# Performance work log

Hardware: AMD Instinct MI355X
Metric: run time of the kernel (lower is better)

## Reference

```python
import jax, jax.numpy as jnp
import numpy as np

EPS = 1e-6


def _mp_match(reps, att, kernel):
    """BiMPM multi-perspective match.
    reps: (B,L,D); att: (B,L,D) or (B,1,D); kernel: (M,D).
    Returns (B,L,1+M): [tanh(sum(reps*att)), tanh(sum_d reps*kernel_m*att)].
    """
    prod = reps * att                                   # (B,L,D)
    cos = jnp.tanh(jnp.sum(prod, axis=-1, keepdims=True))   # (B,L,1)
    mp = jnp.tanh(jnp.einsum('bld,md->blm', prod, kernel))  # (B,L,M)
    return jnp.concatenate([cos, mp], axis=-1)


def setup_inputs() -> dict:
    key = jax.random.key(0)
    ks = jax.random.split(key, 12)
    B, Llt, Lrt, D, M, A = 32, 128, 128, 512, 64, 128
    H = D // 2
    u = lambda k, shape: jax.random.uniform(k, shape, jnp.float32, -0.05, 0.05)  # keras 'uniform' init
    return {
        'reps_lt': jax.random.normal(ks[0], (B, Llt, D), jnp.float32),
        'h_lt_fw': jax.random.normal(ks[1], (B, H), jnp.float32),
        'h_lt_bw': jax.random.normal(ks[2], (B, H), jnp.float32),
        'reps_rt': jax.random.normal(ks[3], (B, Lrt, D), jnp.float32),
        'h_rt_fw': jax.random.normal(ks[4], (B, H), jnp.float32),
        'h_rt_bw': jax.random.normal(ks[5], (B, H), jnp.float32),
        'kernel_full': u(ks[6], (M, D)),
        'kernel_mpool': u(ks[7], (M, D)),
        'attn_w1': u(ks[8], (D, A)),
        'diag_w': u(ks[9], (A,)),
        'kernel_att': u(ks[10], (M, D)),
        'kernel_maxatt': u(ks[11], (M, D)),
    }


def reference(reps_lt, h_lt_fw, h_lt_bw, reps_rt, h_rt_fw, h_rt_bw,
              kernel_full, kernel_mpool, attn_w1, diag_w,
              kernel_att, kernel_maxatt):
    # ---- full match: each left timestep vs last BiLSTM state of right ----
    h_rt = jnp.concatenate([h_rt_fw, h_rt_bw], axis=-1)[:, None, :]  # (B,1,D)
    full = _mp_match(reps_lt, h_rt, kernel_full)                     # (B,Ll,1+M)

    # ---- max-pooling match ----
    # t[b,r,l,m] = tanh(sum_d R[b,r,d]*K[m,d]*L[b,l,d]); max over right positions r
    r_scaled = jnp.einsum('brd,md->brmd', reps_rt, kernel_mpool)     # (B,Lr,M,D)
    t = jnp.tanh(jnp.einsum('brmd,bld->brlm', r_scaled, reps_lt))    # (B,Lr,Ll,M)
    mpool = jnp.max(t, axis=1)                                       # (B,Ll,M)

    # ---- attentive match ----
    a_lt = jnp.tanh(reps_lt @ attn_w1) * diag_w                      # (B,Ll,A)
    a_rt = jnp.tanh(reps_rt @ attn_w1)                               # (B,Lr,A)
    scores = jnp.einsum('bla,bra->blr', a_lt, a_rt)                  # (B,Ll,Lr)
    probs = jax.nn.softmax(scores, axis=-1)
    att = jnp.einsum('blr,brd->bld', probs, reps_rt)                 # (B,Ll,D)
    attentive = _mp_match(reps_lt, att, kernel_att)                  # (B,Ll,1+M)

    # ---- max-attentive match ----
    num = jnp.einsum('bld,brd->blr', reps_lt, reps_rt)
    n_lt = jnp.sqrt(jnp.maximum(jnp.sum(reps_lt * reps_lt, -1), EPS))[:, :, None]
    n_rt = jnp.sqrt(jnp.maximum(jnp.sum(reps_rt * reps_rt, -1), EPS))[:, None, :]
    rel = num / n_rt / n_lt                                          # (B,Ll,Lr)
    idx = jnp.argmax(rel, axis=2)                                    # (B,Ll) int
    max_att = jnp.take_along_axis(reps_rt, idx[:, :, None], axis=1)  # (B,Ll,D)
    maxatt = _mp_match(reps_lt, max_att, kernel_maxatt)              # (B,Ll,1+M)

    return jnp.concatenate([full, mpool, attentive, maxatt], axis=-1)  # (B,Ll,3+4M)
```

## Files before the change

### kernel.cpp

```cpp
#include <hip/hip_runtime.h>
#include <hip/hip_bf16.h>
#include <math.h>
#include <stdint.h>

typedef __attribute__((ext_vector_type(8))) short short8;
typedef __attribute__((ext_vector_type(4))) float float4v;

#define DEV static __device__ __forceinline__

DEV float bflo(unsigned int u) { union { unsigned int i; float f; } v; v.i = u << 16; return v.f; }
DEV float bfhi(unsigned int u) { union { unsigned int i; float f; } v; v.i = u & 0xffff0000u; return v.f; }
DEV unsigned short f2bf(float f) {
    union { float f; unsigned int i; } v; v.f = f;
    unsigned int x = v.i;
    return (unsigned short)((x + 0x7fffu + ((x >> 16) & 1u)) >> 16);
}
DEV unsigned int pack2(float a, float b) { return (unsigned int)f2bf(a) | ((unsigned int)f2bf(b) << 16); }
#if __has_builtin(__builtin_amdgcn_cvt_pk_bf16_f32)
DEV unsigned int pack2_fast(float a, float b) {
    typedef __attribute__((ext_vector_type(2))) short short2v;
    short2v r = __builtin_amdgcn_cvt_pk_bf16_f32(a, b);
    union { short2v s; unsigned int u; } v; v.s = r; return v.u;
}
#else
DEV unsigned int pack2_fast(float a, float b) { return pack2(a, b); }
#endif
DEV void unpack8(uint4 u, float* f) {
    f[0]=bflo(u.x); f[1]=bfhi(u.x); f[2]=bflo(u.y); f[3]=bfhi(u.y);
    f[4]=bflo(u.z); f[5]=bfhi(u.z); f[6]=bflo(u.w); f[7]=bfhi(u.w);
}

DEV void async16(const unsigned short* g, unsigned short* l) {
    __builtin_amdgcn_global_load_lds(
        (const __attribute__((address_space(1))) unsigned int*)g,
        (__attribute__((address_space(3))) unsigned int*)l, 16, 0, 0);
}

__global__ __launch_bounds__(256) void prep_kernel(const float* __restrict__ lt,
                                                   const float* __restrict__ rt,
                                                   const float* __restrict__ kf,
                                                   const float* __restrict__ kmp,
                                                   const float* __restrict__ ka,
                                                   const float* __restrict__ km,
                                                   const float* __restrict__ w1,
                                                   unsigned short* __restrict__ ltb,
                                                   unsigned short* __restrict__ rtb,
                                                   unsigned short* __restrict__ kb,
                                                   unsigned short* __restrict__ w1t,
                                                   double* __restrict__ rsq) {
    __shared__ double ws2[2][2];
    __shared__ float tile[32][33];
    int bid = blockIdx.x, t = threadIdx.x;
    if (bid < 1024) {
        bool isRt = bid >= 512;
        int base = (isRt ? (bid - 512) : bid) * 8;
        int rl = t >> 7;
        int c  = t & 127;
        const float* srcb = isRt ? rt : lt;
        unsigned short* dstb = isRt ? rtb : ltb;
        #pragma unroll
        for (int p = 0; p < 4; ++p) {
            int row = base + p * 2 + rl;
            const float* src = srcb + (size_t)row * 512;
            float4 v = *(const float4*)(src + c * 4);
            ushort4 o;
            o.x = f2bf(v.x); o.y = f2bf(v.y); o.z = f2bf(v.z); o.w = f2bf(v.w);
            *(ushort4*)(dstb + (size_t)row * 512 + c * 4) = o;
            if (isRt) {
                double s = (double)v.x * v.x + (double)v.y * v.y
                         + (double)v.z * v.z + (double)v.w * v.w;
                #pragma unroll
                for (int off = 1; off < 64; off <<= 1) s += __shfl_xor(s, off, 64);
                if ((c & 63) == 0) ws2[rl][c >> 6] = s;
                __syncthreads();
                if (c == 0) rsq[row] = 1.0 / sqrt(ws2[rl][0] + ws2[rl][1]);
                __syncthreads();
            }
        }
    } else if (bid < 1152) {
        int kbk = bid - 1024;
        int ksel = kbk >> 5;
        const float* src = (ksel == 0) ? kf : (ksel == 1) ? kmp : (ksel == 2) ? ka : km;
        int off = (kbk & 31) * 1024 + t * 4;
        float4 v = *(const float4*)(src + off);
        ushort4 o;
        o.x = f2bf(v.x); o.y = f2bf(v.y); o.z = f2bf(v.z); o.w = f2bf(v.w);
        *(ushort4*)(kb + ksel * 32768 + off) = o;
    } else {
        int b2 = bid - 1152;
        int d0 = (b2 & 15) * 32, a0 = (b2 >> 4) * 32;
        int r = t >> 5, c = t & 31;
        #pragma unroll
        for (int i = 0; i < 32; i += 8)
            tile[r + i][c] = w1[(size_t)(d0 + r + i) * 128 + a0 + c];
        __syncthreads();
        #pragma unroll
        for (int i = 0; i < 32; i += 8)
            w1t[(size_t)(a0 + r + i) * 512 + d0 + c] = f2bf(tile[c][r + i]);
    }
}

__global__ __launch_bounds__(256, 3) void uber_kernel(
        const unsigned short* __restrict__ ltb,
        const unsigned short* __restrict__ rtb,
        const unsigned short* __restrict__ kmb,
        const unsigned short* __restrict__ w1t,
        const float* __restrict__ diag,
        unsigned short* __restrict__ a_all,
        const float* __restrict__ ltf,
        const float* __restrict__ rtf,
        const double* __restrict__ rsq,
        int* __restrict__ idxout,
        float* __restrict__ out) {
    __shared__ __align__(16) unsigned char smem[52224];
    int bx = blockIdx.x;
    int t = threadIdx.x;
    int wave = t >> 6, lane = t & 63;
    int q = lane >> 4, col = lane & 15, kq = q * 8;

    if (bx < 2048) {
        int xcd = bx & 7, jj = bx >> 3;
        int b = xcd * 4 + (jj >> 6);
        int m = jj & 63;
        unsigned short (*ltS)[72] = (unsigned short(*)[72])smem;
        unsigned short* rtL = (unsigned short*)(smem + 18432);
        float (*mx)[2] = (float(*)[2])(smem + 18432 + 32768);
        int wl = wave & 1, wr = wave >> 1;
        const unsigned short* ltp = ltb + (size_t)b * 65536;
        const unsigned short* rtp = rtb + (size_t)b * 65536;
        const unsigned short* kr = kmb + (size_t)m * 512;
        int srow = t >> 3, cg8 = t & 7, cg = cg8 * 8;
        int gsw = (cg8 ^ (srow & 7)) * 8;
        int wbase = (t & ~63) * 8;

        #pragma unroll
        for (int it = 0; it < 4; ++it)
            async16(rtp + (size_t)(it * 32 + srow) * 512 + gsw,
                    rtL + it * 2048 + wbase);
        uint4 pk = *(const uint4*)(kr + cg);
        uint4 plt[4];
        #pragma unroll
        for (int it = 0; it < 4; ++it)
            plt[it] = *(const uint4*)(ltp + (size_t)(it * 32 + srow) * 512 + cg);

        float4v acc[4][4] = {};
        for (int k0i = 0; k0i < 8; ++k0i) {
            float kf8[8]; unpack8(pk, kf8);
            #pragma unroll
            for (int it = 0; it < 4; ++it) {
                int row = it * 32 + srow;
                float lf[8]; unpack8(plt[it], lf);
                uint4 s;
                s.x = pack2_fast(lf[0] * kf8[0], lf[1] * kf8[1]);
                s.y = pack2_fast(lf[2] * kf8[2], lf[3] * kf8[3]);
                s.z = pack2_fast(lf[4] * kf8[4], lf[5] * kf8[5]);
                s.w = pack2_fast(lf[6] * kf8[6], lf[7] * kf8[7]);
                *(uint4*)&ltS[row][cg] = s;
            }
            __syncthreads();
            if (k0i < 7) {
                int k0n = (k0i + 1) * 64;
                int bofs = ((k0i + 1) & 1) * 8192;
                #pragma unroll
                for (int it = 0; it < 4; ++it)
                    async16(rtp + (size_t)(it * 32 + srow) * 512 + k0n + gsw,
                            rtL + bofs + it * 2048 + wbase);
                pk = *(const uint4*)(kr + k0n + cg);
                #pragma unroll
                for (int it = 0; it < 4; ++it)
                    plt[it] = *(const uint4*)(ltp + (size_t)(it * 32 + srow) * 512 + k0n + cg);
            }
            const unsigned short* rb = rtL + (k0i & 1) * 8192;
            #pragma unroll
            for (int kk = 0; kk < 64; kk += 32) {
                short8 af[4], bfr[4];
                #pragma unroll
                for (int i = 0; i < 4; ++i)
                    af[i] = *(const short8*)&ltS[wl * 64 + i * 16 + col][kk + kq];
                #pragma unroll
                for (int j = 0; j < 4; ++j) {
                    int row = wr * 64 + j * 16 + col;
                    int slot = ((kk >> 3) + q) ^ (row & 7);
                    bfr[j] = *(const short8*)&rb[row * 64 + slot * 8];
                }
                #pragma unroll
                for (int i = 0; i < 4; ++i)
                    #pragma unroll
                    for (int j = 0; j < 4; ++j)
                        acc[i][j] = __builtin_amdgcn_mfma_f32_16x16x32_bf16(af[i], bfr[j], acc[i][j], 0, 0, 0);
            }
            __syncthreads();
        }
        #pragma unroll
        for (int i = 0; i < 4; ++i)
            #pragma unroll
            for (int ii = 0; ii < 4; ++ii) {
                float v = fmaxf(fmaxf(acc[i][0][ii], acc[i][1][ii]), fmaxf(acc[i][2][ii], acc[i][3][ii]));
                #pragma unroll
                for (int off = 1; off < 16; off <<= 1) v = fmaxf(v, __shfl_xor(v, off, 64));
                if (col == 0) mx[wl * 64 + i * 16 + q * 4 + ii][wr] = v;
            }
        __syncthreads();
        if (t < 128)
            out[((size_t)(b * 128 + t)) * 259 + 65 + m] = tanhf(fmaxf(mx[t][0], mx[t][1]));

    } else if (bx < 2560) {
        int idA = bx - 2048;
        int xcd = idA & 7, jj = idA >> 3;
        int b = xcd * 4 + (jj >> 4);
        int L0 = (jj & 15) * 8;
        float* ltS = (float*)smem;
        float* buf = (float*)(smem + 16384);
        double* dvs = (double*)(smem + 49152);
        float* wv1 = (float*)(smem + 49152 + 128);
        float* wv2 = wv1 + 16;
        int* wi1 = (int*)(wv2 + 16);
        int* wi2 = wi1 + 16;
        int* candi = wi2 + 16;
        {
            int row = t >> 5, c0 = (t & 31) * 16;
            const float* src = ltf + ((size_t)(b * 128 + L0 + row)) * 512 + c0;
            #pragma unroll
            for (int i = 0; i < 4; ++i)
                *(float4*)&ltS[row * 512 + c0 + i * 4] = *(const float4*)(src + i * 4);
        }
        int lg = t >> 7;
        int rg = (t >> 2) & 31;
        int ds = t & 3;
        float acc[4][4] = {{0.f}};
        for (int p = 0; p < 8; ++p) {
            __syncthreads();
            {
                int row = t >> 1, c0 = (t & 1) * 32;
                const float* src = rtf + ((size_t)(b * 128 + row)) * 512 + p * 64 + c0;
                float f[32];
                #pragma unroll
                for (int i = 0; i < 8; ++i)
                    *(float4*)&f[i * 4] = *(const float4*)(src + i * 4);
                int base = row * 64;
                #pragma unroll
                for (int gg = 0; gg < 4; ++gg) {
                    int g = (t & 1) * 4 + gg;
                    int o = ((g ^ (row & 7)) * 8);
                    #pragma unroll
                    for (int k = 0; k < 8; ++k) buf[base + o + k] = f[gg * 8 + k];
                }
            }
            __syncthreads();
            #pragma unroll
            for (int sub = 0; sub < 2; ++sub) {
                int dloc = ds * 16 + sub * 8;
                int dglob = p * 64 + dloc;
                float a[4][8];
                #pragma unroll
                for (int i = 0; i < 4; ++i)
                    #pragma unroll
                    for (int k = 0; k < 8; ++k) a[i][k] = ltS[(lg * 4 + i) * 512 + dglob + k];
                int g = dloc >> 3;
                #pragma unroll
                for (int j = 0; j < 4; ++j) {
                    int r = rg + j * 32;
                    const float* rp = &buf[r * 64 + ((g ^ (r & 7)) * 8)];
                    float rv[8];
                    #pragma unroll
                    for (int k = 0; k < 8; ++k) rv[k] = rp[k];
                    #pragma unroll
                    for (int i = 0; i < 4; ++i)
                        #pragma unroll
                        for (int k = 0; k < 8; ++k)
                            acc[i][j] = fmaf(a[i][k], rv[k], acc[i][j]);
                }
            }
        }
        #pragma unroll
        for (int i = 0; i < 4; ++i)
            #pragma unroll
            for (int j = 0; j < 4; ++j) {
                acc[i][j] += __shfl_xor(acc[i][j], 1, 64);
                acc[i][j] += __shfl_xor(acc[i][j], 2, 64);
            }
        float v1[4], v2[4]; int i1[4], i2[4];
        #pragma unroll
        for (int i = 0; i < 4; ++i) {
            v1[i] = -3.0e38f; v2[i] = -3.0e38f; i1[i] = 0; i2[i] = 1;
            #pragma unroll
            for (int j = 0; j < 4; ++j) {
                int r = rg + j * 32;
                float s = acc[i][j] * (float)rsq[b * 128 + r];
                if (s > v1[i]) { v2[i] = v1[i]; i2[i] = i1[i]; v1[i] = s; i1[i] = r; }
                else if (s > v2[i]) { v2[i] = s; i2[i] = r; }
            }
        }
        #pragma unroll
        for (int off = 4; off < 64; off <<= 1) {
            #pragma unroll
            for (int i = 0; i < 4; ++i) {
                float u1 = __shfl_xor(v1[i], off, 64); int j1 = __shfl_xor(i1[i], off, 64);
                float u2 = __shfl_xor(v2[i], off, 64); int j2 = __shfl_xor(i2[i], off, 64);
                if (u1 > v1[i]) {
                    float ov = v1[i]; int oi = i1[i];
                    v1[i] = u1; i1[i] = j1;
                    if (u2 > ov) { v2[i] = u2; i2[i] = j2; } else { v2[i] = ov; i2[i] = oi; }
                } else if (u1 > v2[i]) { v2[i] = u1; i2[i] = j1; }
            }
        }
        if (lane == 0) {
            #pragma unroll
            for (int i = 0; i < 4; ++i) {
                int l = lg * 4 + i, h = wave & 1;
                wv1[l * 2 + h] = v1[i]; wi1[l * 2 + h] = i1[i];
                wv2[l * 2 + h] = v2[i]; wi2[l * 2 + h] = i2[i];
            }
        }
        __syncthreads();
        if (t < 8) {
            float a1 = wv1[t * 2], a2 = wv2[t * 2]; int ai1 = wi1[t * 2], ai2 = wi2[t * 2];
            float b1 = wv1[t * 2 + 1], b2 = wv2[t * 2 + 1]; int bi1 = wi1[t * 2 + 1], bi2 = wi2[t * 2 + 1];
            int ri1, ri2;
            if (b1 > a1) {
                ri1 = bi1;
                if (b2 > a1) { ri2 = bi2; } else { ri2 = ai1; }
            } else {
                ri1 = ai1;
                if (b1 > a2) { ri2 = bi1; } else { ri2 = ai2; }
            }
            candi[t * 2] = ri1; candi[t * 2 + 1] = ri2;
            (void)a2; (void)b2; (void)ai2; (void)bi2;
        }
        __syncthreads();
        {
            int dotid = t >> 4;
            int sub = t & 15;
            int l = dotid >> 1, c = dotid & 1;
            int r = candi[l * 2 + c];
            const float* lrow = ltf + ((size_t)(b * 128 + L0 + l)) * 512;
            const float* rrow = rtf + ((size_t)(b * 128 + r)) * 512;
            double s = 0.0;
            #pragma unroll 8
            for (int k = 0; k < 32; ++k) {
                int d = sub * 32 + k;
                s = fma((double)lrow[d], (double)rrow[d], s);
            }
            #pragma unroll
            for (int off = 1; off < 16; off <<= 1) s += __shfl_xor(s, off, 64);
            if (sub == 0) dvs[l * 2 + c] = s * rsq[b * 128 + r];
        }
        __syncthreads();
        if (t < 8) {
            int ia = candi[t * 2], ib = candi[t * 2 + 1];
            double va = dvs[t * 2], vb = dvs[t * 2 + 1];
            int res = (vb > va || (vb == va && ib < ia)) ? ib : ia;
            idxout[b * 128 + L0 + t] = res;
        }

    } else {
        int R0 = (bx - 2560) * 32;
        unsigned short (*aS)[72] = (unsigned short(*)[72])smem;
        unsigned short (*bS)[72] = (unsigned short(*)[72])(smem + 4608);
        float* diagS = (float*)(smem + 4608 + 18432);
        int wl = wave & 1, wr = wave >> 1;
        if (t < 128) diagS[t] = diag[t];
        const unsigned short* src = (R0 < 4096) ? (ltb + (size_t)R0 * 512) : (rtb + (size_t)(R0 - 4096) * 512);
        float4v acc[4] = {};
        for (int k0 = 0; k0 < 512; k0 += 64) {
            {
                int row = t >> 3, cg = (t & 7) * 8;
                *(uint4*)&aS[row][cg] = *(const uint4*)(src + (size_t)row * 512 + k0 + cg);
            }
            #pragma unroll
            for (int it = 0; it < 4; ++it) {
                int id = it * 256 + t;
                int row = id >> 3, cg = (id & 7) * 8;
                *(uint4*)&bS[row][cg] = *(const uint4*)(w1t + (size_t)row * 512 + k0 + cg);
            }
            __syncthreads();
            #pragma unroll
            for (int kk = 0; kk < 64; kk += 32) {
                short8 af = *(const short8*)&aS[wl * 16 + col][kk + kq];
                #pragma unroll
                for (int j = 0; j < 4; ++j) {
                    short8 bf = *(const short8*)&bS[wr * 64 + j * 16 + col][kk + kq];
                    acc[j] = __builtin_amdgcn_mfma_f32_16x16x32_bf16(af, bf, acc[j], 0, 0, 0);
                }
            }
            __syncthreads();
        }
        bool isLt = (R0 < 4096);
        #pragma unroll
        for (int j = 0; j < 4; ++j)
            #pragma unroll
            for (int ii = 0; ii < 4; ++ii) {
                int rowl = wl * 16 + q * 4 + ii;
                int n = wr * 64 + j * 16 + col;
                float v = tanhf(acc[j][ii]);
                if (isLt) v *= diagS[n];
                a_all[((size_t)(R0 + rowl)) * 128 + n] = f2bf(v);
            }
    }
}

__global__ __launch_bounds__(512, 1) void attn_kernel(const unsigned short* __restrict__ a_all,
                                                      const unsigned short* __restrict__ rtb,
                                                      const float* __restrict__ ltf,
                                                      const unsigned short* __restrict__ kb_att,
                                                      float* __restrict__ out) {
    int b = blockIdx.x, lg = blockIdx.y;
    int L0 = lg * 16;
    __shared__ __align__(16) unsigned short altS[16][136];
    __shared__ __align__(16) unsigned short artS[128][136];
    __shared__ __align__(16) unsigned short rtS[16][512];
    __shared__ __align__(16) unsigned short prodsF[16][520];
    __shared__ float P[16][132];
    __shared__ float pmax[16][8];
    __shared__ float psum[16][8];
    int t = threadIdx.x;
    int wave = t >> 6, lane = t & 63;
    int q = lane >> 4, col = lane & 15, kq = q * 8;

    if (t < 256) {
        int row = t >> 4, c0 = (t & 15) * 8;
        *(uint4*)&altS[row][c0] = *(const uint4*)(a_all + ((size_t)(b * 128 + L0 + row)) * 128 + c0);
    }
    {
        int row = t >> 2, c0 = (t & 3) * 32;
        const unsigned short* src = a_all + ((size_t)(4096 + b * 128 + row)) * 128 + c0;
        #pragma unroll
        for (int i = 0; i < 4; ++i)
            *(uint4*)&artS[row][c0 + i * 8] = *(const uint4*)(src + i * 8);
    }
    __syncthreads();

    float4v acc = {};
    #pragma unroll
    for (int kk = 0; kk < 128; kk += 32) {
        short8 af = *(const short8*)&altS[col][kk + kq];
        short8 bf = *(const short8*)&artS[wave * 16 + col][kk + kq];
        acc = __builtin_amdgcn_mfma_f32_16x16x32_bf16(af, bf, acc, 0, 0, 0);
    }
    float m4[4], p4[4];
    #pragma unroll
    for (int ii = 0; ii < 4; ++ii) {
        float v = acc[ii];
        #pragma unroll
        for (int off = 1; off < 16; off <<= 1) v = fmaxf(v, __shfl_xor(v, off, 64));
        m4[ii] = v;
    }
    if (col == 0) {
        #pragma unroll
        for (int ii = 0; ii < 4; ++ii) pmax[q * 4 + ii][wave] = m4[ii];
    }
    __syncthreads();
    #pragma unroll
    for (int ii = 0; ii < 4; ++ii) {
        float M = pmax[q * 4 + ii][0];
        #pragma unroll
        for (int w = 1; w < 8; ++w) M = fmaxf(M, pmax[q * 4 + ii][w]);
        p4[ii] = expf(acc[ii] - M);
        float s = p4[ii];
        #pragma unroll
        for (int off = 1; off < 16; off <<= 1) s += __shfl_xor(s, off, 64);
        m4[ii] = s;
    }
    if (col == 0) {
        #pragma unroll
        for (int ii = 0; ii < 4; ++ii) psum[q * 4 + ii][wave] = m4[ii];
    }
    __syncthreads();
    #pragma unroll
    for (int ii = 0; ii < 4; ++ii) {
        float S = psum[q * 4 + ii][0] + psum[q * 4 + ii][1] + psum[q * 4 + ii][2] + psum[q * 4 + ii][3]
                + psum[q * 4 + ii][4] + psum[q * 4 + ii][5] + psum[q * 4 + ii][6] + psum[q * 4 + ii][7];
        P[q * 4 + ii][wave * 16 + col] = p4[ii] / S;
    }

    int l = t >> 5, cd = t & 31;
    float a8[2][8] = {{0.f}};
    for (int rcb = 0; rcb < 128; rcb += 16) {
        __syncthreads();
        {
            int row = t >> 5, c0 = (t & 31) * 16;
            const unsigned short* src = rtb + ((size_t)(b * 128 + rcb + row)) * 512 + c0;
            *(uint4*)&rtS[row][c0] = *(const uint4*)src;
            *(uint4*)&rtS[row][c0 + 8] = *(const uint4*)(src + 8);
        }
        __syncthreads();
        for (int rr = 0; rr < 16; ++rr) {
            float pr = P[l][rcb + rr];
            #pragma unroll
            for (int pass = 0; pass < 2; ++pass) {
                uint4 u = *(const uint4*)&rtS[rr][pass * 256 + cd * 8];
                float f[8]; unpack8(u, f);
                #pragma unroll
                for (int k = 0; k < 8; ++k) a8[pass][k] += pr * f[k];
            }
        }
    }

    int grow = b * 128 + L0 + l;
    const float* ltrow = ltf + (size_t)grow * 512;
    float csum = 0.f;
    #pragma unroll
    for (int pass = 0; pass < 2; ++pass) {
        int d0 = pass * 256 + cd * 8;
        float lf[8];
        *(float4*)&lf[0] = *(const float4*)(ltrow + d0);
        *(float4*)&lf[4] = *(const float4*)(ltrow + d0 + 4);
        float pf[8];
        #pragma unroll
        for (int k = 0; k < 8; ++k) { pf[k] = lf[k] * a8[pass][k]; csum += pf[k]; }
        uint4 o;
        o.x = pack2(pf[0], pf[1]); o.y = pack2(pf[2], pf[3]);
        o.z = pack2(pf[4], pf[5]); o.w = pack2(pf[6], pf[7]);
        *(uint4*)&prodsF[l][d0] = o;
    }
    #pragma unroll
    for (int off = 1; off < 32; off <<= 1) csum += __shfl_xor(csum, off, 64);
    if (cd == 0) out[(size_t)grow * 259 + 129] = tanhf(csum);

    unsigned short* Ks = &artS[0][0];
    float* red = (float*)&rtS[0][0];
    for (int half = 0; half < 2; ++half) {
        __syncthreads();
        {
            int row = t >> 4, c0 = (t & 15) * 32;
            const unsigned short* src = kb_att + ((size_t)(half * 32 + row)) * 512 + c0;
            #pragma unroll
            for (int i = 0; i < 4; ++i)
                *(uint4*)&Ks[row * 520 + c0 + i * 8] = *(const uint4*)(src + i * 8);
        }
        __syncthreads();
        float4v pacc[2] = {};
        #pragma unroll
        for (int kk = 0; kk < 64; kk += 32) {
            short8 af = *(const short8*)&prodsF[col][wave * 64 + kk + kq];
            #pragma unroll
            for (int j = 0; j < 2; ++j) {
                short8 bf = *(const short8*)&Ks[(j * 16 + col) * 520 + wave * 64 + kk + kq];
                pacc[j] = __builtin_amdgcn_mfma_f32_16x16x32_bf16(af, bf, pacc[j], 0, 0, 0);
            }
        }
        #pragma unroll
        for (int j = 0; j < 2; ++j)
            #pragma unroll
            for (int ii = 0; ii < 4; ++ii)
                red[((wave * 2 + j) * 16 + q * 4 + ii) * 16 + col] = pacc[j][ii];
        __syncthreads();
        {
            int ll = t >> 5, jm = t & 31;
            int j = jm >> 4, mc = jm & 15;
            float s = 0.f;
            #pragma unroll
            for (int w = 0; w < 8; ++w) s += red[((w * 2 + j) * 16 + ll) * 16 + mc];
            out[((size_t)(b * 128 + L0 + ll)) * 259 + 130 + half * 32 + jm] = tanhf(s);
        }
    }
}

__global__ __launch_bounds__(256, 2) void mpmatch_kernel(const float* __restrict__ lt,
                                                         const unsigned short* __restrict__ rtb,
                                                         const float* __restrict__ hfw,
                                                         const float* __restrict__ hbw,
                                                         const unsigned short* __restrict__ kb,
                                                         const int* __restrict__ idxp,
                                                         float* __restrict__ out) {
    int lg = blockIdx.x, b = blockIdx.y, mode = blockIdx.z ? 2 : 0;
    int L0 = lg * 16;
    __shared__ __align__(16) unsigned short prods[16][520];
    __shared__ __align__(16) unsigned short Ks[32][520];
    __shared__ float red[4][2][16][17];
    int t = threadIdx.x;
    int wave = t >> 6, lane = t & 63;
    int q = lane >> 4, col = lane & 15, kq = q * 8;

    const unsigned short* Kp = kb + (size_t)((mode == 0) ? 0 : 3 * 32768);
    int obase = (mode == 0) ? 0 : 194;

    int l = t >> 4, c = t & 15;
    int grow = b * 128 + L0 + l;
    const float* ltrow = lt + (size_t)grow * 512;
    const unsigned short* avrow = 0;
    if (mode == 2) avrow = rtb + ((size_t)(b * 128 + idxp[grow])) * 512;

    float csum = 0.f;
    #pragma unroll
    for (int pass = 0; pass < 4; ++pass) {
        int d0 = pass * 128 + c * 8;
        float lf[8], af[8], pf[8];
        *(float4*)&lf[0] = *(const float4*)(ltrow + d0);
        *(float4*)&lf[4] = *(const float4*)(ltrow + d0 + 4);
        if (mode == 0) {
            const float* h = (d0 < 256) ? (hfw + b * 256 + d0) : (hbw + b * 256 + d0 - 256);
            *(float4*)&af[0] = *(const float4*)h;
            *(float4*)&af[4] = *(const float4*)(h + 4);
        } else {
            uint4 av = *(const uint4*)(avrow + d0);
            unpack8(av, af);
        }
        #pragma unroll
        for (int k = 0; k < 8; ++k) { pf[k] = lf[k] * af[k]; csum += pf[k]; }
        uint4 o;
        o.x = pack2(pf[0], pf[1]); o.y = pack2(pf[2], pf[3]);
        o.z = pack2(pf[4], pf[5]); o.w = pack2(pf[6], pf[7]);
        *(uint4*)&prods[l][d0] = o;
    }
    #pragma unroll
    for (int off = 1; off < 16; off <<= 1) csum += __shfl_xor(csum, off, 64);
    if (c == 0) out[(size_t)grow * 259 + obase] = tanhf(csum);

    for (int half = 0; half < 2; ++half) {
        {
            int row = t >> 3, c0 = (t & 7) * 64;
            const unsigned short* src = Kp + ((size_t)(half * 32 + row)) * 512 + c0;
            #pragma unroll
            for (int i = 0; i < 8; ++i)
                *(uint4*)&Ks[row][c0 + i * 8] = *(const uint4*)(src + i * 8);
        }
        __syncthreads();
        float4v acc[2] = {};
        #pragma unroll
        for (int kk = 0; kk < 128; kk += 32) {
            short8 af = *(const short8*)&prods[col][wave * 128 + kk + kq];
            #pragma unroll
            for (int j = 0; j < 2; ++j) {
                short8 bf = *(const short8*)&Ks[j * 16 + col][wave * 128 + kk + kq];
                acc[j] = __builtin_amdgcn_mfma_f32_16x16x32_bf16(af, bf, acc[j], 0, 0, 0);
            }
        }
        #pragma unroll
        for (int j = 0; j < 2; ++j)
            #pragma unroll
            for (int ii = 0; ii < 4; ++ii)
                red[wave][j][q * 4 + ii][col] = acc[j][ii];
        __syncthreads();
        for (int o = t; o < 512; o += 256) {
            int ll = o >> 5, jm = o & 31;
            int j = jm >> 4, mc = jm & 15;
            float s = red[0][j][ll][mc] + red[1][j][ll][mc] + red[2][j][ll][mc] + red[3][j][ll][mc];
            out[((size_t)(b * 128 + L0 + ll)) * 259 + obase + 1 + half * 32 + jm] = tanhf(s);
        }
        __syncthreads();
    }
}

extern "C" void kernel_launch(void* const* d_in, const int* in_sizes, int n_in,
                              void* d_out, int out_size, void* d_ws, size_t ws_size,
                              hipStream_t stream) {
    const float* lt  = (const float*)d_in[0];
    const float* rt  = (const float*)d_in[3];
    const float* hfw = (const float*)d_in[4];
    const float* hbw = (const float*)d_in[5];
    const float* kf  = (const float*)d_in[6];
    const float* kmp = (const float*)d_in[7];
    const float* w1  = (const float*)d_in[8];
    const float* dia = (const float*)d_in[9];
    const float* ka  = (const float*)d_in[10];
    const float* km  = (const float*)d_in[11];
    float* out = (float*)d_out;

    char* wsb = (char*)d_ws;
    unsigned short* ltb16 = (unsigned short*)(wsb);
    unsigned short* rtb16 = (unsigned short*)(wsb + 4194304);
    unsigned short* kb16  = (unsigned short*)(wsb + 8388608);
    unsigned short* w1t   = (unsigned short*)(wsb + 8650752);
    unsigned short* a_all = (unsigned short*)(wsb + 8781824);
    double*         rsq   = (double*)(wsb + 15073280);
    int*            idx   = (int*)(wsb + 15106048);

    prep_kernel<<<1216, 256, 0, stream>>>(lt, rt, kf, kmp, ka, km, w1, ltb16, rtb16, kb16, w1t, rsq);
    uber_kernel<<<2816, 256, 0, stream>>>(ltb16, rtb16, kb16 + 32768, w1t, dia, a_all,
                                          lt, rt, rsq, idx, out);
    attn_kernel<<<dim3(32, 8), 512, 0, stream>>>(a_all, rtb16, lt, kb16 + 2 * 32768, out);
    mpmatch_kernel<<<dim3(8, 32, 2), 256, 0, stream>>>(lt, rtb16, hfw, hbw, kb16, idx, out);
}
```

Before: 196.8 us.

## Merge attention and mp-match kernels into one tail launch; compute rt norms locally

Folds attn_kernel and mpmatch_kernel into a single tail_kernel that dispatches on block index, so one launch replaces two. The mp-match half now uses 512 threads and computes both 32-wide M halves in one pass. Each max-attentive block now recomputes the right-row inverse norms in shared memory, which removes the double-precision reduction and its syncs from prep_kernel. The cost is redundant norm work, a serial per-thread double loop of 256 elements, and a larger shared-memory footprint for the merged kernel.

```diff
diff --git a/kernel.cpp b/kernel.cpp
--- a/kernel.cpp
+++ b/kernel.cpp
@@ -46,9 +46,7 @@
                                                    unsigned short* __restrict__ ltb,
                                                    unsigned short* __restrict__ rtb,
                                                    unsigned short* __restrict__ kb,
-                                                   unsigned short* __restrict__ w1t,
-                                                   double* __restrict__ rsq) {
-    __shared__ double ws2[2][2];
+                                                   unsigned short* __restrict__ w1t) {
     __shared__ float tile[32][33];
     int bid = blockIdx.x, t = threadIdx.x;
     if (bid < 1024) {
@@ -66,16 +64,6 @@
             ushort4 o;
             o.x = f2bf(v.x); o.y = f2bf(v.y); o.z = f2bf(v.z); o.w = f2bf(v.w);
             *(ushort4*)(dstb + (size_t)row * 512 + c * 4) = o;
-            if (isRt) {
-                double s = (double)v.x * v.x + (double)v.y * v.y
-                         + (double)v.z * v.z + (double)v.w * v.w;
-                #pragma unroll
-                for (int off = 1; off < 64; off <<= 1) s += __shfl_xor(s, off, 64);
-                if ((c & 63) == 0) ws2[rl][c >> 6] = s;
-                __syncthreads();
-                if (c == 0) rsq[row] = 1.0 / sqrt(ws2[rl][0] + ws2[rl][1]);
-                __syncthreads();
-            }
         }
     } else if (bid < 1152) {
         int kbk = bid - 1024;
@@ -109,7 +97,6 @@
         unsigned short* __restrict__ a_all,
         const float* __restrict__ ltf,
         const float* __restrict__ rtf,
-        const double* __restrict__ rsq,
         int* __restrict__ idxout,
         float* __restrict__ out) {
     __shared__ __align__(16) unsigned char smem[52224];
@@ -217,12 +204,22 @@
         int* wi1 = (int*)(wv2 + 16);
         int* wi2 = wi1 + 16;
         int* candi = wi2 + 16;
+        double* rsqS = (double*)(smem + 50176);
         {
             int row = t >> 5, c0 = (t & 31) * 16;
             const float* src = ltf + ((size_t)(b * 128 + L0 + row)) * 512 + c0;
             #pragma unroll
             for (int i = 0; i < 4; ++i)
                 *(float4*)&ltS[row * 512 + c0 + i * 4] = *(const float4*)(src + i * 4);
+        }
+        {
+            int r = t >> 1, half = t & 1;
+            const float* rrow = rtf + ((size_t)(b * 128 + r)) * 512 + half * 256;
+            double s = 0.0;
+            #pragma unroll 4
+            for (int k = 0; k < 256; ++k) s = fma((double)rrow[k], (double)rrow[k], s);
+            s += __shfl_xor(s, 1, 64);
+            if (half == 0) rsqS[r] = 1.0 / sqrt(s);
         }
         int lg = t >> 7;
         int rg = (t >> 2) & 31;
@@ -286,7 +283,7 @@
             #pragma unroll
             for (int j = 0; j < 4; ++j) {
                 int r = rg + j * 32;
-                float s = acc[i][j] * (float)rsq[b * 128 + r];
+                float s = acc[i][j] * (float)rsqS[r];
                 if (s > v1[i]) { v2[i] = v1[i]; i2[i] = i1[i]; v1[i] = s; i1[i] = r; }
                 else if (s > v2[i]) { v2[i] = s; i2[i] = r; }
             }
@@ -343,7 +340,7 @@
             }
             #pragma unroll
             for (int off = 1; off < 16; off <<= 1) s += __shfl_xor(s, off, 64);
-            if (sub == 0) dvs[l * 2 + c] = s * rsq[b * 128 + r];
+            if (sub == 0) dvs[l * 2 + c] = s * rsqS[r];
         }
         __syncthreads();
         if (t < 8) {
@@ -399,246 +396,251 @@
     }
 }
 
-__global__ __launch_bounds__(512, 1) void attn_kernel(const unsigned short* __restrict__ a_all,
-                                                      const unsigned short* __restrict__ rtb,
-                                                      const float* __restrict__ ltf,
-                                                      const unsigned short* __restrict__ kb_att,
-                                                      float* __restrict__ out) {
-    int b = blockIdx.x, lg = blockIdx.y;
-    int L0 = lg * 16;
-    __shared__ __align__(16) unsigned short altS[16][136];
-    __shared__ __align__(16) unsigned short artS[128][136];
-    __shared__ __align__(16) unsigned short rtS[16][512];
-    __shared__ __align__(16) unsigned short prodsF[16][520];
-    __shared__ float P[16][132];
-    __shared__ float pmax[16][8];
-    __shared__ float psum[16][8];
+__global__ __launch_bounds__(512, 1) void tail_kernel(
+        const unsigned short* __restrict__ a_all,
+        const unsigned short* __restrict__ rtb,
+        const float* __restrict__ ltf,
+        const unsigned short* __restrict__ kb,
+        const float* __restrict__ hfw,
+        const float* __restrict__ hbw,
+        const int* __restrict__ idxp,
+        float* __restrict__ out) {
+    __shared__ __align__(16) unsigned char smem[99584];
+    int bx = blockIdx.x;
     int t = threadIdx.x;
     int wave = t >> 6, lane = t & 63;
     int q = lane >> 4, col = lane & 15, kq = q * 8;
 
-    if (t < 256) {
-        int row = t >> 4, c0 = (t & 15) * 8;
-        *(uint4*)&altS[row][c0] = *(const uint4*)(a_all + ((size_t)(b * 128 + L0 + row)) * 128 + c0);
-    }
-    {
-        int row = t >> 2, c0 = (t & 3) * 32;
-        const unsigned short* src = a_all + ((size_t)(4096 + b * 128 + row)) * 128 + c0;
-        #pragma unroll
-        for (int i = 0; i < 4; ++i)
-            *(uint4*)&artS[row][c0 + i * 8] = *(const uint4*)(src + i * 8);
-    }
-    __syncthreads();
-
-    float4v acc = {};
-    #pragma unroll
-    for (int kk = 0; kk < 128; kk += 32) {
-        short8 af = *(const short8*)&altS[col][kk + kq];
-        short8 bf = *(const short8*)&artS[wave * 16 + col][kk + kq];
-        acc = __builtin_amdgcn_mfma_f32_16x16x32_bf16(af, bf, acc, 0, 0, 0);
-    }
-    float m4[4], p4[4];
-    #pragma unroll
-    for (int ii = 0; ii < 4; ++ii) {
-        float v = acc[ii];
-        #pragma unroll
-        for (int off = 1; off < 16; off <<= 1) v = fmaxf(v, __shfl_xor(v, off, 64));
-        m4[ii] = v;
-    }
-    if (col == 0) {
-        #pragma unroll
-        for (int ii = 0; ii < 4; ++ii) pmax[q * 4 + ii][wave] = m4[ii];
-    }
-    __syncthreads();
-    #pragma unroll
-    for (int ii = 0; ii < 4; ++ii) {
-        float M = pmax[q * 4 + ii][0];
-        #pragma unroll
-        for (int w = 1; w < 8; ++w) M = fmaxf(M, pmax[q * 4 + ii][w]);
-        p4[ii] = expf(acc[ii] - M);
-        float s = p4[ii];
-        #pragma unroll
-        for (int off = 1; off < 16; off <<= 1) s += __shfl_xor(s, off, 64);
-        m4[ii] = s;
-    }
-    if (col == 0) {
-        #pragma unroll
-        for (int ii = 0; ii < 4; ++ii) psum[q * 4 + ii][wave] = m4[ii];
-    }
-    __syncthreads();
-    #pragma unroll
-    for (int ii = 0; ii < 4; ++ii) {
-        float S = psum[q * 4 + ii][0] + psum[q * 4 + ii][1] + psum[q * 4 + ii][2] + psum[q * 4 + ii][3]
-                + psum[q * 4 + ii][4] + psum[q * 4 + ii][5] + psum[q * 4 + ii][6] + psum[q * 4 + ii][7];
-        P[q * 4 + ii][wave * 16 + col] = p4[ii] / S;
-    }
-
-    int l = t >> 5, cd = t & 31;
-    float a8[2][8] = {{0.f}};
-    for (int rcb = 0; rcb < 128; rcb += 16) {
-        __syncthreads();
+    if (bx < 256) {
+        int b = bx & 31, lg = bx >> 5;
+        int L0 = lg * 16;
+        unsigned short (*altS)[136]  = (unsigned short(*)[136])(smem);
+        unsigned short (*artS)[136]  = (unsigned short(*)[136])(smem + 4352);
+        unsigned short (*rtS)[512]   = (unsigned short(*)[512])(smem + 39168);
+        unsigned short (*prodsF)[520]= (unsigned short(*)[520])(smem + 55552);
+        float (*P)[132]  = (float(*)[132])(smem + 72192);
+        float (*pmax)[8] = (float(*)[8])(smem + 80640);
+        float (*psum)[8] = (float(*)[8])(smem + 81152);
+        const unsigned short* kb_att = kb + 2 * 32768;
+
+        if (t < 256) {
+            int row = t >> 4, c0 = (t & 15) * 8;
+            *(uint4*)&altS[row][c0] = *(const uint4*)(a_all + ((size_t)(b * 128 + L0 + row)) * 128 + c0);
+        }
         {
-            int row = t >> 5, c0 = (t & 31) * 16;
-            const unsigned short* src = rtb + ((size_t)(b * 128 + rcb + row)) * 512 + c0;
-            *(uint4*)&rtS[row][c0] = *(const uint4*)src;
-            *(uint4*)&rtS[row][c0 + 8] = *(const uint4*)(src + 8);
-        }
-        __syncthreads();
-        for (int rr = 0; rr < 16; ++rr) {
-            float pr = P[l][rcb + rr];
-            #pragma unroll
-            for (int pass = 0; pass < 2; ++pass) {
-                uint4 u = *(const uint4*)&rtS[rr][pass * 256 + cd * 8];
-                float f[8]; unpack8(u, f);
-                #pragma unroll
-                for (int k = 0; k < 8; ++k) a8[pass][k] += pr * f[k];
-            }
-        }
-    }
-
-    int grow = b * 128 + L0 + l;
-    const float* ltrow = ltf + (size_t)grow * 512;
-    float csum = 0.f;
-    #pragma unroll
-    for (int pass = 0; pass < 2; ++pass) {
-        int d0 = pass * 256 + cd * 8;
-        float lf[8];
-        *(float4*)&lf[0] = *(const float4*)(ltrow + d0);
-        *(float4*)&lf[4] = *(const float4*)(ltrow + d0 + 4);
-        float pf[8];
-        #pragma unroll
-        for (int k = 0; k < 8; ++k) { pf[k] = lf[k] * a8[pass][k]; csum += pf[k]; }
-        uint4 o;
-        o.x = pack2(pf[0], pf[1]); o.y = pack2(pf[2], pf[3]);
-        o.z = pack2(pf[4], pf[5]); o.w = pack2(pf[6], pf[7]);
-        *(uint4*)&prodsF[l][d0] = o;
-    }
-    #pragma unroll
-    for (int off = 1; off < 32; off <<= 1) csum += __shfl_xor(csum, off, 64);
-    if (cd == 0) out[(size_t)grow * 259 + 129] = tanhf(csum);
-
-    unsigned short* Ks = &artS[0][0];
-    float* red = (float*)&rtS[0][0];
-    for (int half = 0; half < 2; ++half) {
-        __syncthreads();
+            int row = t >> 2, c0 = (t & 3) * 32;
+            const unsigned short* src = a_all + ((size_t)(4096 + b * 128 + row)) * 128 + c0;
+            #pragma unroll
+            for (int i = 0; i < 4; ++i)
+                *(uint4*)&artS[row][c0 + i * 8] = *(const uint4*)(src + i * 8);
+        }
+        __syncthreads();
+
+        float4v acc = {};
+        #pragma unroll
+        for (int kk = 0; kk < 128; kk += 32) {
+            short8 af = *(const short8*)&altS[col][kk + kq];
+            short8 bf = *(const short8*)&artS[wave * 16 + col][kk + kq];
+            acc = __builtin_amdgcn_mfma_f32_16x16x32_bf16(af, bf, acc, 0, 0, 0);
+        }
+        float m4[4], p4[4];
+        #pragma unroll
+        for (int ii = 0; ii < 4; ++ii) {
+            float v = acc[ii];
+            #pragma unroll
+            for (int off = 1; off < 16; off <<= 1) v = fmaxf(v, __shfl_xor(v, off, 64));
+            m4[ii] = v;
+        }
+        if (col == 0) {
+            #pragma unroll
+            for (int ii = 0; ii < 4; ++ii) pmax[q * 4 + ii][wave] = m4[ii];
+        }
+        __syncthreads();
+        #pragma unroll
+        for (int ii = 0; ii < 4; ++ii) {
+            float M = pmax[q * 4 + ii][0];
+            #pragma unroll
+            for (int w = 1; w < 8; ++w) M = fmaxf(M, pmax[q * 4 + ii][w]);
+            p4[ii] = expf(acc[ii] - M);
+            float s = p4[ii];
+            #pragma unroll
+            for (int off = 1; off < 16; off <<= 1) s += __shfl_xor(s, off, 64);
+            m4[ii] = s;
+        }
+        if (col == 0) {
+            #pragma unroll
+            for (int ii = 0; ii < 4; ++ii) psum[q * 4 + ii][wave] = m4[ii];
+        }
+        __syncthreads();
+        #pragma unroll
+        for (int ii = 0; ii < 4; ++ii) {
+            float S = psum[q * 4 + ii][0] + psum[q * 4 + ii][1] + psum[q * 4 + ii][2] + psum[q * 4 + ii][3]
+                    + psum[q * 4 + ii][4] + psum[q * 4 + ii][5] + psum[q * 4 + ii][6] + psum[q * 4 + ii][7];
+            P[q * 4 + ii][wave * 16 + col] = p4[ii] / S;
+        }
+
+        int l = t >> 5, cd = t & 31;
+        float a8[2][8] = {{0.f}};
+        for (int rcb = 0; rcb < 128; rcb += 16) {
+            __syncthreads();
+            {
+                int row = t >> 5, c0 = (t & 31) * 16;
+                const unsigned short* src = rtb + ((size_t)(b * 128 + rcb + row)) * 512 + c0;
+                *(uint4*)&rtS[row][c0] = *(const uint4*)src;
+                *(uint4*)&rtS[row][c0 + 8] = *(const uint4*)(src + 8);
+            }
+            __syncthreads();
+            for (int rr = 0; rr < 16; ++rr) {
+                float pr = P[l][rcb + rr];
+                #pragma unroll
+                for (int pass = 0; pass < 2; ++pass) {
+                    uint4 u = *(const uint4*)&rtS[rr][pass * 256 + cd * 8];
+                    float f[8]; unpack8(u, f);
+                    #pragma unroll
+                    for (int k = 0; k < 8; ++k) a8[pass][k] += pr * f[k];
+                }
+            }
+        }
+
+        int grow = b * 128 + L0 + l;
+        const float* ltrow = ltf + (size_t)grow * 512;
+        float csum = 0.f;
+        #pragma unroll
+        for (int pass = 0; pass < 2; ++pass) {
+            int d0 = pass * 256 + cd * 8;
+            float lf[8];
+            *(float4*)&lf[0] = *(const float4*)(ltrow + d0);
+            *(float4*)&lf[4] = *(const float4*)(ltrow + d0 + 4);
+            float pf[8];
+            #pragma unroll
+            for (int k = 0; k < 8; ++k) { pf[k] = lf[k] * a8[pass][k]; csum += pf[k]; }
+            uint4 o;
+            o.x = pack2(pf[0], pf[1]); o.y = pack2(pf[2], pf[3]);
+            o.z = pack2(pf[4], pf[5]); o.w = pack2(pf[6], pf[7]);
+            *(uint4*)&prodsF[l][d0] = o;
+        }
+        #pragma unroll
+        for (int off = 1; off < 32; off <<= 1) csum += __shfl_xor(csum, off, 64);
+        if (cd == 0) out[(size_t)grow * 259 + 129] = tanhf(csum);
+
+        unsigned short* Ks = &artS[0][0];
+        float* red = (float*)&rtS[0][0];
+        for (int half = 0; half < 2; ++half) {
+            __syncthreads();
+            {
+                int row = t >> 4, c0 = (t & 15) * 32;
+                const unsigned short* src = kb_att + ((size_t)(half * 32 + row)) * 512 + c0;
+                #pragma unroll
+                for (int i = 0; i < 4; ++i)
+                    *(uint4*)&Ks[row * 520 + c0 + i * 8] = *(const uint4*)(src + i * 8);
+            }
+            __syncthreads();
+            float4v pacc[2] = {};
+            #pragma unroll
+            for (int kk = 0; kk < 64; kk += 32) {
+                short8 af = *(const short8*)&prodsF[col][wave * 64 + kk + kq];
+                #pragma unroll
+                for (int j = 0; j < 2; ++j) {
+                    short8 bf = *(const short8*)&Ks[(j * 16 + col) * 520 + wave * 64 + kk + kq];
+                    pacc[j] = __builtin_amdgcn_mfma_f32_16x16x32_bf16(af, bf, pacc[j], 0, 0, 0);
+                }
+            }
+            #pragma unroll
+            for (int j = 0; j < 2; ++j)
+                #pragma unroll
+                for (int ii = 0; ii < 4; ++ii)
+                    red[((wave * 2 + j) * 16 + q * 4 + ii) * 16 + col] = pacc[j][ii];
+            __syncthreads();
+            {
+                int ll = t >> 5, jm = t & 31;
+                int j = jm >> 4, mc = jm & 15;
+                float s = 0.f;
+                #pragma unroll
+                for (int w = 0; w < 8; ++w) s += red[((w * 2 + j) * 16 + ll) * 16 + mc];
+                out[((size_t)(b * 128 + L0 + ll)) * 259 + 130 + half * 32 + jm] = tanhf(s);
+            }
+        }
+
+    } else {
+        int idB = bx - 256;
+        int lg = idB & 7, b = (idB >> 3) & 31;
+        int mode = (idB >> 8) ? 2 : 0;
+        int L0 = lg * 16;
+        unsigned short (*prods)[520] = (unsigned short(*)[520])smem;
+        unsigned short* Ks = (unsigned short*)(smem + 16640);
+        float* red = (float*)(smem + 83200);
+        const unsigned short* Kp = kb + (size_t)((mode == 0) ? 0 : 3 * 32768);
+        int obase = (mode == 0) ? 0 : 194;
+
+        if (t < 256) {
+            int l = t >> 4, c = t & 15;
+            int grow = b * 128 + L0 + l;
+            const float* ltrow = ltf + (size_t)grow * 512;
+            const unsigned short* avrow = 0;
+            if (mode == 2) avrow = rtb + ((size_t)(b * 128 + idxp[grow])) * 512;
+            float csum = 0.f;
+            #pragma unroll
+            for (int pass = 0; pass < 4; ++pass) {
+                int d0 = pass * 128 + c * 8;
+                float lf[8], af[8], pf[8];
+                *(float4*)&lf[0] = *(const float4*)(ltrow + d0);
+                *(float4*)&lf[4] = *(const float4*)(ltrow + d0 + 4);
+                if (mode == 0) {
+                    const float* h = (d0 < 256) ? (hfw + b * 256 + d0) : (hbw + b * 256 + d0 - 256);
+                    *(float4*)&af[0] = *(const float4*)h;
+                    *(float4*)&af[4] = *(const float4*)(h + 4);
+                } else {
+                    uint4 av = *(const uint4*)(avrow + d0);
+                    unpack8(av, af);
+                }
+                #pragma unroll
+                for (int k = 0; k < 8; ++k) { pf[k] = lf[k] * af[k]; csum += pf[k]; }
+                uint4 o;
+                o.x = pack2(pf[0], pf[1]); o.y = pack2(pf[2], pf[3]);
+                o.z = pack2(pf[4], pf[5]); o.w = pack2(pf[6], pf[7]);
+                *(uint4*)&prods[l][d0] = o;
+            }
+            #pragma unroll
+            for (int off = 1; off < 16; off <<= 1) csum += __shfl_xor(csum, off, 64);
+            if (c == 0) out[(size_t)grow * 259 + obase] = tanhf(csum);
+        }
         {
-            int row = t >> 4, c0 = (t & 15) * 32;
-            const unsigned short* src = kb_att + ((size_t)(half * 32 + row)) * 512 + c0;
-            #pragma unroll
-            for (int i = 0; i < 4; ++i)
+            int row = t >> 3, c0 = (t & 7) * 64;
+            const unsigned short* src = Kp + (size_t)row * 512 + c0;
+            #pragma unroll
+            for (int i = 0; i < 8; ++i)
                 *(uint4*)&Ks[row * 520 + c0 + i * 8] = *(const uint4*)(src + i * 8);
         }
         __syncthreads();
-        float4v pacc[2] = {};
-        #pragma unroll
-        for (int kk = 0; kk < 64; kk += 32) {
-            short8 af = *(const short8*)&prodsF[col][wave * 64 + kk + kq];
+        int hs = wave >> 2, w4 = wave & 3;
+        float4v acc2[2] = {};
+        #pragma unroll
+        for (int kk = 0; kk < 128; kk += 32) {
+            short8 af = *(const short8*)&prods[col][w4 * 128 + kk + kq];
             #pragma unroll
             for (int j = 0; j < 2; ++j) {
-                short8 bf = *(const short8*)&Ks[(j * 16 + col) * 520 + wave * 64 + kk + kq];
-                pacc[j] = __builtin_amdgcn_mfma_f32_16x16x32_bf16(af, bf, pacc[j], 0, 0, 0);
+                short8 bf = *(const short8*)&Ks[(size_t)(hs * 32 + j * 16 + col) * 520 + w4 * 128 + kk + kq];
+                acc2[j] = __builtin_amdgcn_mfma_f32_16x16x32_bf16(af, bf, acc2[j], 0, 0, 0);
             }
         }
         #pragma unroll
         for (int j = 0; j < 2; ++j)
             #pragma unroll
             for (int ii = 0; ii < 4; ++ii)
-                red[((wave * 2 + j) * 16 + q * 4 + ii) * 16 + col] = pacc[j][ii];
-        __syncthreads();
-        {
-            int ll = t >> 5, jm = t & 31;
+                red[(((hs * 4 + w4) * 2 + j) * 16 + (q * 4 + ii)) * 16 + col] = acc2[j][ii];
+        __syncthreads();
+        #pragma unroll
+        for (int o = 0; o < 2; ++o) {
+            int oo = t + o * 512;
+            int ll = oo >> 6;
+            int rem = oo & 63;
+            int hh = rem >> 5, jm = rem & 31;
             int j = jm >> 4, mc = jm & 15;
             float s = 0.f;
             #pragma unroll
-            for (int w = 0; w < 8; ++w) s += red[((w * 2 + j) * 16 + ll) * 16 + mc];
-            out[((size_t)(b * 128 + L0 + ll)) * 259 + 130 + half * 32 + jm] = tanhf(s);
-        }
-    }
-}
-
-__global__ __launch_bounds__(256, 2) void mpmatch_kernel(const float* __restrict__ lt,
-                                                         const unsigned short* __restrict__ rtb,
-                                                         const float* __restrict__ hfw,
-                                                         const float* __restrict__ hbw,
-                                                         const unsigned short* __restrict__ kb,
-                                                         const int* __restrict__ idxp,
-                                                         float* __restrict__ out) {
-    int lg = blockIdx.x, b = blockIdx.y, mode = blockIdx.z ? 2 : 0;
-    int L0 = lg * 16;
-    __shared__ __align__(16) unsigned short prods[16][520];
-    __shared__ __align__(16) unsigned short Ks[32][520];
-    __shared__ float red[4][2][16][17];
-    int t = threadIdx.x;
-    int wave = t >> 6, lane = t & 63;
-    int q = lane >> 4, col = lane & 15, kq = q * 8;
-
-    const unsigned short* Kp = kb + (size_t)((mode == 0) ? 0 : 3 * 32768);
-    int obase = (mode == 0) ? 0 : 194;
-
-    int l = t >> 4, c = t & 15;
-    int grow = b * 128 + L0 + l;
-    const float* ltrow = lt + (size_t)grow * 512;
-    const unsigned short* avrow = 0;
-    if (mode == 2) avrow = rtb + ((size_t)(b * 128 + idxp[grow])) * 512;
-
-    float csum = 0.f;
-    #pragma unroll
-    for (int pass = 0; pass < 4; ++pass) {
-        int d0 = pass * 128 + c * 8;
-        float lf[8], af[8], pf[8];
-        *(float4*)&lf[0] = *(const float4*)(ltrow + d0);
-        *(float4*)&lf[4] = *(const float4*)(ltrow + d0 + 4);
-        if (mode == 0) {
-            const float* h = (d0 < 256) ? (hfw + b * 256 + d0) : (hbw + b * 256 + d0 - 256);
-            *(float4*)&af[0] = *(const float4*)h;
-            *(float4*)&af[4] = *(const float4*)(h + 4);
-        } else {
-            uint4 av = *(const uint4*)(avrow + d0);
-            unpack8(av, af);
-        }
-        #pragma unroll
-        for (int k = 0; k < 8; ++k) { pf[k] = lf[k] * af[k]; csum += pf[k]; }
-        uint4 o;
-        o.x = pack2(pf[0], pf[1]); o.y = pack2(pf[2], pf[3]);
-        o.z = pack2(pf[4], pf[5]); o.w = pack2(pf[6], pf[7]);
-        *(uint4*)&prods[l][d0] = o;
-    }
-    #pragma unroll
-    for (int off = 1; off < 16; off <<= 1) csum += __shfl_xor(csum, off, 64);
-    if (c == 0) out[(size_t)grow * 259 + obase] = tanhf(csum);
-
-    for (int half = 0; half < 2; ++half) {
-        {
-            int row = t >> 3, c0 = (t & 7) * 64;
-            const unsigned short* src = Kp + ((size_t)(half * 32 + row)) * 512 + c0;
-            #pragma unroll
-            for (int i = 0; i < 8; ++i)
-                *(uint4*)&Ks[row][c0 + i * 8] = *(const uint4*)(src + i * 8);
-        }
-        __syncthreads();
-        float4v acc[2] = {};
-        #pragma unroll
-        for (int kk = 0; kk < 128; kk += 32) {
-            short8 af = *(const short8*)&prods[col][wave * 128 + kk + kq];
-            #pragma unroll
-            for (int j = 0; j < 2; ++j) {
-                short8 bf = *(const short8*)&Ks[j * 16 + col][wave * 128 + kk + kq];
-                acc[j] = __builtin_amdgcn_mfma_f32_16x16x32_bf16(af, bf, acc[j], 0, 0, 0);
-            }
-        }
-        #pragma unroll
-        for (int j = 0; j < 2; ++j)
-            #pragma unroll
-            for (int ii = 0; ii < 4; ++ii)
-                red[wave][j][q * 4 + ii][col] = acc[j][ii];
-        __syncthreads();
-        for (int o = t; o < 512; o += 256) {
-            int ll = o >> 5, jm = o & 31;
-            int j = jm >> 4, mc = jm & 15;
-            float s = red[0][j][ll][mc] + red[1][j][ll][mc] + red[2][j][ll][mc] + red[3][j][ll][mc];
-            out[((size_t)(b * 128 + L0 + ll)) * 259 + obase + 1 + half * 32 + jm] = tanhf(s);
-        }
-        __syncthreads();
+            for (int w = 0; w < 4; ++w) s += red[(((hh * 4 + w) * 2 + j) * 16 + ll) * 16 + mc];
+            out[((size_t)(b * 128 + L0 + ll)) * 259 + obase + 1 + hh * 32 + jm] = tanhf(s);
+        }
     }
 }
 
@@ -663,12 +665,10 @@
     unsigned short* kb16  = (unsigned short*)(wsb + 8388608);
     unsigned short* w1t   = (unsigned short*)(wsb + 8650752);
     unsigned short* a_all = (unsigned short*)(wsb + 8781824);
-    double*         rsq   = (double*)(wsb + 15073280);
     int*            idx   = (int*)(wsb + 15106048);
 
-    prep_kernel<<<1216, 256, 0, stream>>>(lt, rt, kf, kmp, ka, km, w1, ltb16, rtb16, kb16, w1t, rsq);
+    prep_kernel<<<1216, 256, 0, stream>>>(lt, rt, kf, kmp, ka, km, w1, ltb16, rtb16, kb16, w1t);
     uber_kernel<<<2816, 256, 0, stream>>>(ltb16, rtb16, kb16 + 32768, w1t, dia, a_all,
-                                          lt, rt, rsq, idx, out);
-    attn_kernel<<<dim3(32, 8), 512, 0, stream>>>(a_all, rtb16, lt, kb16 + 2 * 32768, out);
-    mpmatch_kernel<<<dim3(8, 32, 2), 256, 0, stream>>>(lt, rtb16, hfw, hbw, kb16, idx, out);
-}
+                                          lt, rt, idx, out);
+    tail_kernel<<<768, 512, 0, stream>>>(a_all, rtb16, lt, kb16, hfw, hbw, idx, out);
+}
```

Measured after the change: 219.1 us. +11.3%, slower.
